# Kernel tuning notes

Hardware: AMD Instinct MI355X
Metric: run time of the kernel (lower is better)

Reference implementation:

```python
import jax, jax.numpy as jnp
import numpy as np

B, P, G, C = 32, 8192, 150, 8
ALPHA, GAMMA, W_ASPECT = 0.25, 2.0, 1.0
THRESH = 1.5          # current_epoch = 0  (< 5)
COST_W_DIST, COST_W_CLS = 2.0, 0.5  # current_epoch < 10
EPS = 1e-6


def _boxes(key, shape):
    k1, k2 = jax.random.split(key)
    c = jax.random.uniform(k1, shape + (2,), minval=0.1, maxval=0.9)
    s = jax.random.uniform(k2, shape + (2,), minval=0.01, maxval=0.2)
    return jnp.concatenate([c - s / 2, c + s / 2], axis=-1)  # valid xyxy


def setup_inputs() -> dict:
    key = jax.random.key(0)
    ks = jax.random.split(key, 6)
    return {
        "pred_objectness": jax.random.uniform(ks[0], (B, P), dtype=jnp.float32),
        "pred_bboxes": _boxes(ks[1], (B, P)),
        "pred_class_logits": jax.random.normal(ks[2], (B, P, C), dtype=jnp.float32),
        "gt_bboxes": _boxes(ks[3], (B, G)),
        "gt_labels": jax.random.randint(ks[4], (B, G), 0, C),
        "num_objects": jax.random.randint(ks[5], (B,), 1, G),
    }


def _giou(b1, b2):
    # elementwise over broadcastable [..., 4] boxes
    a1 = (b1[..., 2] - b1[..., 0]) * (b1[..., 3] - b1[..., 1])
    a2 = (b2[..., 2] - b2[..., 0]) * (b2[..., 3] - b2[..., 1])
    iw = jnp.clip(jnp.minimum(b1[..., 2], b2[..., 2]) - jnp.maximum(b1[..., 0], b2[..., 0]), 0.0)
    ih = jnp.clip(jnp.minimum(b1[..., 3], b2[..., 3]) - jnp.maximum(b1[..., 1], b2[..., 1]), 0.0)
    inter = iw * ih
    union = a1 + a2 - inter
    iou = inter / (union + EPS)
    enc = (jnp.maximum(b1[..., 2], b2[..., 2]) - jnp.minimum(b1[..., 0], b2[..., 0])) * \
          (jnp.maximum(b1[..., 3], b2[..., 3]) - jnp.minimum(b1[..., 1], b2[..., 1]))
    return iou - (enc - union) / (enc + EPS)


def _focal(p, t):
    p = jnp.clip(p, 1e-7, 1.0 - 1e-7)
    bce = -(t * jnp.log(p) + (1.0 - t) * jnp.log(1.0 - p))
    pt = p * t + (1.0 - p) * (1.0 - t)
    return jnp.mean(ALPHA * (1.0 - pt) ** GAMMA * bce)


def _per_image(obj, pbox, plog, gbox, glbl, n_obj):
    gt_mask = jnp.arange(G) < n_obj                              # [G]
    pc = (pbox[:, :2] + pbox[:, 2:]) / 2
    gc = (gbox[:, :2] + gbox[:, 2:]) / 2
    d2 = jnp.sum((pc[:, None, :] - gc[None, :, :]) ** 2, axis=-1)  # [P,G]
    norm_dist = jnp.sqrt(jnp.clip(d2, 1e-12)) / jnp.sqrt(2.0)
    giou_m = _giou(pbox[:, None, :], gbox[None, :, :])           # [P,G]
    probs = jax.nn.softmax(plog, axis=-1)                        # [P,C]
    cls_cost = -probs[:, glbl]                                   # [P,G]
    cost = COST_W_DIST * norm_dist - giou_m + COST_W_CLS * cls_cost
    min_cost = cost.min(axis=0)                                  # per-gt best pred
    assigned = cost.argmin(axis=0)                               # [G]
    valid = (min_cost < THRESH) & gt_mask
    # conflict resolution: for each pred, keep the lowest-cost gt assigned to it
    M = valid[None, :] & (assigned[None, :] == jnp.arange(P)[:, None])  # [P,G]
    matched = M.any(axis=1)                                      # [P]
    best_gt = jnp.where(M, cost, jnp.inf).argmin(axis=1)         # [P]
    wm = matched.astype(cost.dtype)
    n_m = wm.sum()
    denom = jnp.maximum(n_m, 1.0)
    obj_loss = _focal(obj, wm)
    mg = gbox[best_gt]                                           # [P,4]
    giou_loss = jnp.sum(wm * (1.0 - _giou(pbox, mg))) / denom
    pa = (pbox[:, 2] - pbox[:, 0]) / (pbox[:, 3] - pbox[:, 1] + EPS)
    ga = (mg[:, 2] - mg[:, 0]) / (mg[:, 3] - mg[:, 1] + EPS)
    da = jnp.abs(pa - ga)
    sl1 = jnp.where(da < 1.0, 0.5 * da * da, da - 0.5)
    aspect_loss = jnp.sum(wm * sl1) / denom
    lsm = jax.nn.log_softmax(plog, axis=-1)
    ce = -lsm[jnp.arange(P), glbl[best_gt]]
    class_loss = jnp.sum(wm * ce) / denom
    return obj_loss, giou_loss + W_ASPECT * aspect_loss, class_loss, n_m


def reference(pred_objectness, pred_bboxes, pred_class_logits, gt_bboxes, gt_labels, num_objects):
    o, bb, cl, nm = jax.vmap(_per_image)(pred_objectness, pred_bboxes, pred_class_logits,
                                         gt_bboxes, gt_labels, num_objects)
    denom = jnp.maximum(nm.sum(), 1.0)
    obj_loss = o.mean()
    bbox_loss = bb.sum() / denom
    class_loss = cl.sum() / denom
    total_loss = obj_loss + bbox_loss + class_loss
    return total_loss, obj_loss, bbox_loss, class_loss
```

## Files before the change

kernel.cpp:

```cpp
#include <hip/hip_runtime.h>
#include <math.h>

namespace {
constexpr int B_ = 32, P_ = 8192, G_ = 150, C_ = 8;
constexpr int TG = 10;
constexpr int NTILE = G_ / TG;
constexpr int PCH = 16;
constexpr int PCHUNK = P_ / PCH;
constexpr int NXCD = 8;
constexpr int LT = 1024;
constexpr float ALPHA_ = 0.25f;
constexpr float THRESH_ = 1.5f;
constexpr float EPS_ = 1e-6f;
constexpr float LOG2E_ = 1.44269504088896340736f;
constexpr float LN2_   = 0.69314718055994530942f;
constexpr float HSQ2_ = 0.70710678118654752440f;
}

__device__ __forceinline__ float rcp_f(float x) { return __builtin_amdgcn_rcpf(x); }
__device__ __forceinline__ float rfl_f(float x) {
    return __int_as_float(__builtin_amdgcn_readfirstlane(__float_as_int(x)));
}

__device__ __forceinline__ float giou_f(const float4 b1, const float4 b2) {
    float a1 = (b1.z - b1.x) * (b1.w - b1.y);
    float a2 = (b2.z - b2.x) * (b2.w - b2.y);
    float iw = fmaxf(fminf(b1.z, b2.z) - fmaxf(b1.x, b2.x), 0.0f);
    float ih = fmaxf(fminf(b1.w, b2.w) - fmaxf(b1.y, b2.y), 0.0f);
    float inter = iw * ih;
    float uni = a1 + a2 - inter;
    float iou = inter / (uni + EPS_);
    float enc = (fmaxf(b1.z, b2.z) - fminf(b1.x, b2.x)) *
                (fmaxf(b1.w, b2.w) - fminf(b1.y, b2.y));
    return iou - (enc - uni) / (enc + EPS_);
}

__device__ __forceinline__ float block_sum1024(float v, const int tid) {
    __shared__ float tmp[LT / 64];
    for (int off = 32; off; off >>= 1) v += __shfl_down(v, off, 64);
    if ((tid & 63) == 0) tmp[tid >> 6] = v;
    __syncthreads();
    float r = 0.0f;
#pragma unroll
    for (int i = 0; i < LT / 64; ++i) r += tmp[i];
    __syncthreads();
    return r;
}

__global__ __launch_bounds__(64) void k_cost_min(
    const float* __restrict__ pbox,
    const float* __restrict__ plog,
    const float* __restrict__ gbox,
    const int*   __restrict__ glbl,
    const int*   __restrict__ nobj,
    float* __restrict__ out_minc,
    int*   __restrict__ out_assig,
    int*   __restrict__ cnt)
{
    if (blockIdx.x == 0 && threadIdx.x == 0) *cnt = 0;

    const int bid  = blockIdx.x;
    const int xcd  = bid & (NXCD - 1);
    const int t2   = bid >> 3;
    const int tile = t2 % NTILE;
    const int grp  = t2 / NTILE;
    const int pair = xcd + NXCD * grp;
    const int ch   = pair & (PCH - 1);
    const int b    = pair >> 4;
    const int g0   = tile * TG;
    if (g0 >= nobj[b]) return;

    const int tid = threadIdx.x;
    const int p0  = ch * PCHUNK;

    __shared__ float sw[64][9];

    float gx1[TG], gy1[TG], gx2[TG], gy2[TG], gcx[TG], gcy[TG], gar[TG];
    int gL[TG];
    {
        const float4* gb4 = (const float4*)(gbox + ((size_t)b * G_ + g0) * 4);
        const int* gl = glbl + b * G_ + g0;
#pragma unroll
        for (int j = 0; j < TG; ++j) {
            const float4 gb = gb4[j];
            gx1[j] = rfl_f(gb.x); gy1[j] = rfl_f(gb.y);
            gx2[j] = rfl_f(gb.z); gy2[j] = rfl_f(gb.w);
            gcx[j] = rfl_f((gb.x + gb.z) * HSQ2_);
            gcy[j] = rfl_f((gb.y + gb.w) * HSQ2_);
            gar[j] = rfl_f((gb.z - gb.x) * (gb.w - gb.y));
            gL[j]  = __builtin_amdgcn_readfirstlane(gl[j]);
        }
    }

    float bc[TG]; int bi[TG];
#pragma unroll
    for (int j = 0; j < TG; ++j) { bc[j] = INFINITY; bi[j] = 0; }

    const float4* pb4 = (const float4*)(pbox + (size_t)b * P_ * 4);
    const float4* pl4 = (const float4*)(plog + (size_t)b * P_ * C_);

    for (int p = p0 + tid; p < p0 + PCHUNK; p += 64) {
        const float4 pb = pb4[p];
        const float4 l0 = pl4[2 * p];
        const float4 l1 = pl4[2 * p + 1];
        const float pcx = (pb.x + pb.z) * HSQ2_;
        const float pcy = (pb.y + pb.w) * HSQ2_;
        const float a1  = (pb.z - pb.x) * (pb.w - pb.y);

        const float m = fmaxf(fmaxf(fmaxf(l0.x, l0.y), fmaxf(l0.z, l0.w)),
                              fmaxf(fmaxf(l1.x, l1.y), fmaxf(l1.z, l1.w)));
        const float mm = -m * LOG2E_;
        const float e0 = __builtin_amdgcn_exp2f(fmaf(l0.x, LOG2E_, mm));
        const float e1 = __builtin_amdgcn_exp2f(fmaf(l0.y, LOG2E_, mm));
        const float e2 = __builtin_amdgcn_exp2f(fmaf(l0.z, LOG2E_, mm));
        const float e3 = __builtin_amdgcn_exp2f(fmaf(l0.w, LOG2E_, mm));
        const float e4 = __builtin_amdgcn_exp2f(fmaf(l1.x, LOG2E_, mm));
        const float e5 = __builtin_amdgcn_exp2f(fmaf(l1.y, LOG2E_, mm));
        const float e6 = __builtin_amdgcn_exp2f(fmaf(l1.z, LOG2E_, mm));
        const float e7 = __builtin_amdgcn_exp2f(fmaf(l1.w, LOG2E_, mm));
        const float se = ((e0 + e1) + (e2 + e3)) + ((e4 + e5) + (e6 + e7));
        const float s  = -0.5f * rcp_f(se);
        sw[tid][0] = e0 * s; sw[tid][1] = e1 * s; sw[tid][2] = e2 * s; sw[tid][3] = e3 * s;
        sw[tid][4] = e4 * s; sw[tid][5] = e5 * s; sw[tid][6] = e6 * s; sw[tid][7] = e7 * s;

#pragma unroll
        for (int j = 0; j < TG; ++j) {
            const float dx = pcx - gcx[j], dy = pcy - gcy[j];
            const float d2 = fmaf(dx, dx, dy * dy);
            const float sd = __builtin_amdgcn_sqrtf(d2);

            const float iwr = fminf(pb.z, gx2[j]) - fmaxf(pb.x, gx1[j]);
            const float ihr = fminf(pb.w, gy2[j]) - fmaxf(pb.y, gy1[j]);
            const float inter = fmaxf(iwr, 0.0f) * fmaxf(ihr, 0.0f);
            const float uni = (a1 + gar[j]) - inter;
            const float encw = (fmaxf(pb.z, gx2[j]) - fminf(pb.x, gx1[j]));
            const float ench = (fmaxf(pb.w, gy2[j]) - fminf(pb.y, gy1[j]));
            const float enc  = encw * ench;
            const float x = uni + EPS_;
            const float y = enc + EPS_;
            const float r = rcp_f(x * y);
            const float num = fmaf(enc - uni, x, -(inter * y));
            const float c0 = num * r;
            const float cost = sd + (c0 + sw[tid][gL[j]]);
            if (cost < bc[j]) { bc[j] = cost; bi[j] = p; }
        }
    }

#pragma unroll
    for (int j = 0; j < TG; ++j) {
        float c = bc[j]; int i = bi[j];
        for (int off = 32; off; off >>= 1) {
            const float c2 = __shfl_down(c, off, 64);
            const int   i2 = __shfl_down(i, off, 64);
            if (c2 < c || (c2 == c && i2 < i)) { c = c2; i = i2; }
        }
        if (tid == 0) {
            out_minc[(b * G_ + g0 + j) * PCH + ch]  = c;
            out_assig[(b * G_ + g0 + j) * PCH + ch] = i;
        }
    }
}

__global__ __launch_bounds__(LT) void k_losses(
    const float* __restrict__ obj,
    const float* __restrict__ pbox,
    const float* __restrict__ plog,
    const float* __restrict__ gbox,
    const int*   __restrict__ glbl,
    const int*   __restrict__ nobj,
    const float* __restrict__ pminc,
    const int*   __restrict__ passig,
    float* __restrict__ img,
    int* __restrict__ cnt,
    float* __restrict__ out)
{
    const int b = blockIdx.x, tid = threadIdx.x;
    __shared__ float s_c[G_];
    __shared__ int   s_p[G_];
    __shared__ unsigned char s_valid[G_], s_win[G_];
    __shared__ int s_wp[G_], s_wg[G_], s_nw;
    __shared__ int s_last;

    const int n = nobj[b];
    if (tid < G_) {
        float c = INFINITY; int i = 0x7fffffff;
        const float* pc = pminc  + (size_t)(b * G_ + tid) * PCH;
        const int*   pi = passig + (size_t)(b * G_ + tid) * PCH;
#pragma unroll
        for (int ch = 0; ch < PCH; ++ch) {
            const float c2 = pc[ch]; const int i2 = pi[ch];
            if (c2 < c || (c2 == c && i2 < i)) { c = c2; i = i2; }
        }
        s_c[tid] = c;
        s_p[tid] = i;
        s_valid[tid] = (c < THRESH_) && (tid < n);
    }
    __syncthreads();

    if (tid < G_) {
        unsigned char w = 0;
        if (s_valid[tid]) {
            w = 1;
            const int p = s_p[tid]; const float c = s_c[tid];
            for (int g2 = 0; g2 < G_; ++g2) {
                if (g2 == tid || !s_valid[g2] || s_p[g2] != p) continue;
                const float c2 = s_c[g2];
                if (c2 < c || (c2 == c && g2 < tid)) { w = 0; break; }
            }
        }
        s_win[tid] = w;
    }
    __syncthreads();
    if (tid == 0) {
        int nw = 0;
        for (int g = 0; g < G_; ++g) nw += s_win[g];
        s_nw = nw;
    }
    if (tid < G_ && s_win[tid]) {
        int slot = 0;
        for (int g2 = 0; g2 < tid; ++g2) slot += s_win[g2];
        s_wp[slot] = s_p[tid];
        s_wg[slot] = tid;
    }
    __syncthreads();
    const int nw = s_nw;

    const float* ob = obj + (size_t)b * P_;
    float fsum = 0.0f;
#pragma unroll
    for (int k = 0; k < P_ / LT; ++k) {
        float v = ob[tid + k * LT];
        v = fminf(fmaxf(v, 1e-7f), 1.0f - 1e-7f);
        const float nl = -__builtin_amdgcn_logf(1.0f - v) * LN2_;
        fsum += ALPHA_ * v * v * nl;
    }

    float gsum = 0.0f, asum = 0.0f, csum = 0.0f;
    if (tid < nw) {
        const int p = s_wp[tid], g = s_wg[tid];
        float v = ob[p];
        v = fminf(fmaxf(v, 1e-7f), 1.0f - 1e-7f);
        const float nl1 = -__builtin_amdgcn_logf(1.0f - v) * LN2_;
        fsum += ALPHA_ * (1.0f - v) * (1.0f - v) * (-logf(v))
              - ALPHA_ * v * v * nl1;

        const float4 pb = *(const float4*)(pbox + ((size_t)b * P_ + p) * 4);
        const float4 gb = *(const float4*)(gbox + ((size_t)b * G_ + g) * 4);
        gsum = 1.0f - giou_f(pb, gb);

        const float pa = (pb.z - pb.x) / (pb.w - pb.y + EPS_);
        const float ga = (gb.z - gb.x) / (gb.w - gb.y + EPS_);
        const float da = fabsf(pa - ga);
        asum = (da < 1.0f) ? 0.5f * da * da : (da - 0.5f);

        const float* lg = plog + ((size_t)b * P_ + p) * C_;
        const float l0 = lg[0], l1 = lg[1], l2 = lg[2], l3 = lg[3];
        const float l4 = lg[4], l5 = lg[5], l6 = lg[6], l7 = lg[7];
        const float m = fmaxf(fmaxf(fmaxf(l0, l1), fmaxf(l2, l3)),
                              fmaxf(fmaxf(l4, l5), fmaxf(l6, l7)));
        const float se = expf(l0 - m) + expf(l1 - m) + expf(l2 - m) + expf(l3 - m)
                       + expf(l4 - m) + expf(l5 - m) + expf(l6 - m) + expf(l7 - m);
        const int L = glbl[b * G_ + g];
        const float lL = lg[L];
        csum = -(lL - m - logf(se));
    }

    const float ft  = block_sum1024(fsum, tid);
    const float gt_ = block_sum1024(gsum, tid);
    const float at  = block_sum1024(asum, tid);
    const float ct  = block_sum1024(csum, tid);

    if (tid == 0) {
        const float denom = fmaxf((float)nw, 1.0f);
        img[b * 4 + 0] = ft / (float)P_;
        img[b * 4 + 1] = gt_ / denom + at / denom;
        img[b * 4 + 2] = ct / denom;
        img[b * 4 + 3] = (float)nw;
        __threadfence();
        const int old = atomicAdd(cnt, 1);
        s_last = (old == B_ - 1);
    }
    __syncthreads();
    if (tid == 0 && s_last) {
        __threadfence();
        float so = 0.f, sbb = 0.f, scl = 0.f, snm = 0.f;
        for (int bb2 = 0; bb2 < B_; ++bb2) {
            so  += img[bb2 * 4 + 0];
            sbb += img[bb2 * 4 + 1];
            scl += img[bb2 * 4 + 2];
            snm += img[bb2 * 4 + 3];
        }
        const float denom = fmaxf(snm, 1.0f);
        const float o  = so / (float)B_;
        const float bb = sbb / denom;
        const float cl = scl / denom;
        out[0] = o + bb + cl;
        out[1] = o;
        out[2] = bb;
        out[3] = cl;
        *cnt = 0;
    }
}

extern "C" void kernel_launch(void* const* d_in, const int* in_sizes, int n_in,
                              void* d_out, int out_size, void* d_ws, size_t ws_size,
                              hipStream_t stream) {
    const float* obj  = (const float*)d_in[0];
    const float* pbox = (const float*)d_in[1];
    const float* plog = (const float*)d_in[2];
    const float* gbox = (const float*)d_in[3];
    const int*   glbl = (const int*)d_in[4];
    const int*   nobj = (const int*)d_in[5];
    float* out = (float*)d_out;

    char* ws = (char*)d_ws;
    size_t off = 0;
    float* pminc  = (float*)(ws + off); off += (size_t)B_ * G_ * PCH * 4;
    int*   passig = (int*)  (ws + off); off += (size_t)B_ * G_ * PCH * 4;
    float* img    = (float*)(ws + off); off += (size_t)B_ * 4 * 4;
    int*   cnt    = (int*)  (ws + off); off += 64;

    k_cost_min<<<dim3(NTILE * PCH * B_), 64, 0, stream>>>(pbox, plog, gbox, glbl,
                                                          nobj, pminc, passig, cnt);
    k_losses<<<dim3(B_), LT, 0, stream>>>(obj, pbox, plog, gbox, glbl, nobj,
                                          pminc, passig, img, cnt, out);
}
```

Baseline: 75.68 us.

## Parallelize winner resolution, fuse block reductions, vectorize objectness loads in loss kernel

The loss kernel drops from 1024 to 512 threads per block. The serial 150-way per-GT conflict scan is split across 8 sub-slices per GT, and the winning GTs are recorded in a shared bitmask, so slot prefix sums use popcount instead of linear loops. The four separate block reductions become one float4 reduction with a single sync pair, and objectness values are read as float4. The goal is to shorten the serial, single-thread parts of this single-wave-per-image kernel. The cost is an extra barrier and shared atomics.

```diff
diff --git a/kernel.cpp b/kernel.cpp
--- a/kernel.cpp
+++ b/kernel.cpp
@@ -8,7 +8,7 @@
 constexpr int PCH = 16;
 constexpr int PCHUNK = P_ / PCH;
 constexpr int NXCD = 8;
-constexpr int LT = 1024;
+constexpr int LT = 512;
 constexpr float ALPHA_ = 0.25f;
 constexpr float THRESH_ = 1.5f;
 constexpr float EPS_ = 1e-6f;
@@ -35,15 +35,24 @@
     return iou - (enc - uni) / (enc + EPS_);
 }
 
-__device__ __forceinline__ float block_sum1024(float v, const int tid) {
-    __shared__ float tmp[LT / 64];
-    for (int off = 32; off; off >>= 1) v += __shfl_down(v, off, 64);
-    if ((tid & 63) == 0) tmp[tid >> 6] = v;
-    __syncthreads();
-    float r = 0.0f;
-#pragma unroll
-    for (int i = 0; i < LT / 64; ++i) r += tmp[i];
-    __syncthreads();
+__device__ __forceinline__ float4 block_sum4(float4 v, const int tid) {
+    __shared__ float tmp[LT / 64][4];
+    for (int o = 32; o; o >>= 1) {
+        v.x += __shfl_down(v.x, o, 64);
+        v.y += __shfl_down(v.y, o, 64);
+        v.z += __shfl_down(v.z, o, 64);
+        v.w += __shfl_down(v.w, o, 64);
+    }
+    const int wv = tid >> 6;
+    if ((tid & 63) == 0) {
+        tmp[wv][0] = v.x; tmp[wv][1] = v.y; tmp[wv][2] = v.z; tmp[wv][3] = v.w;
+    }
+    __syncthreads();
+    float4 r = make_float4(0.f, 0.f, 0.f, 0.f);
+#pragma unroll
+    for (int i = 0; i < LT / 64; ++i) {
+        r.x += tmp[i][0]; r.y += tmp[i][1]; r.z += tmp[i][2]; r.w += tmp[i][3];
+    }
     return r;
 }
 
@@ -177,12 +186,15 @@
     const int b = blockIdx.x, tid = threadIdx.x;
     __shared__ float s_c[G_];
     __shared__ int   s_p[G_];
-    __shared__ unsigned char s_valid[G_], s_win[G_];
+    __shared__ unsigned char s_valid[G_], s_beat[G_];
+    __shared__ unsigned int s_winm[5];
     __shared__ int s_wp[G_], s_wg[G_], s_nw;
     __shared__ int s_last;
 
     const int n = nobj[b];
+    if (tid < 5) s_winm[tid] = 0;
     if (tid < G_) {
+        s_beat[tid] = 0;
         float c = INFINITY; int i = 0x7fffffff;
         const float* pc = pminc  + (size_t)(b * G_ + tid) * PCH;
         const int*   pi = passig + (size_t)(b * G_ + tid) * PCH;
@@ -197,28 +209,38 @@
     }
     __syncthreads();
 
+    for (int t = tid; t < G_ * 8; t += LT) {
+        const int g  = t >> 3;
+        const int sl = t & 7;
+        if (!s_valid[g]) continue;
+        const int p = s_p[g]; const float c = s_c[g];
+        const int g2e = min(sl * 19 + 19, G_);
+        for (int g2 = sl * 19; g2 < g2e; ++g2) {
+            if (g2 == g || !s_valid[g2] || s_p[g2] != p) continue;
+            const float c2 = s_c[g2];
+            if (c2 < c || (c2 == c && g2 < g)) { s_beat[g] = 1; break; }
+        }
+    }
+    __syncthreads();
+
     if (tid < G_) {
-        unsigned char w = 0;
-        if (s_valid[tid]) {
-            w = 1;
-            const int p = s_p[tid]; const float c = s_c[tid];
-            for (int g2 = 0; g2 < G_; ++g2) {
-                if (g2 == tid || !s_valid[g2] || s_p[g2] != p) continue;
-                const float c2 = s_c[g2];
-                if (c2 < c || (c2 == c && g2 < tid)) { w = 0; break; }
-            }
-        }
-        s_win[tid] = w;
-    }
-    __syncthreads();
+        if (s_valid[tid] && !s_beat[tid])
+            atomicOr(&s_winm[tid >> 5], 1u << (tid & 31));
+    }
+    __syncthreads();
+
     if (tid == 0) {
         int nw = 0;
-        for (int g = 0; g < G_; ++g) nw += s_win[g];
+#pragma unroll
+        for (int w2 = 0; w2 < 5; ++w2) nw += __popc(s_winm[w2]);
         s_nw = nw;
     }
-    if (tid < G_ && s_win[tid]) {
-        int slot = 0;
-        for (int g2 = 0; g2 < tid; ++g2) slot += s_win[g2];
+    if (tid < G_ && s_valid[tid] && !s_beat[tid]) {
+        const int word = tid >> 5, bit = tid & 31;
+        int slot = __popc(s_winm[word] & ((1u << bit) - 1));
+#pragma unroll
+        for (int w2 = 0; w2 < 4; ++w2)
+            if (w2 < word) slot += __popc(s_winm[w2]);
         s_wp[slot] = s_p[tid];
         s_wg[slot] = tid;
     }
@@ -226,13 +248,18 @@
     const int nw = s_nw;
 
     const float* ob = obj + (size_t)b * P_;
+    const float4* ob4 = (const float4*)ob;
     float fsum = 0.0f;
 #pragma unroll
-    for (int k = 0; k < P_ / LT; ++k) {
-        float v = ob[tid + k * LT];
-        v = fminf(fmaxf(v, 1e-7f), 1.0f - 1e-7f);
-        const float nl = -__builtin_amdgcn_logf(1.0f - v) * LN2_;
-        fsum += ALPHA_ * v * v * nl;
+    for (int k = 0; k < P_ / (LT * 4); ++k) {
+        const float4 v4 = ob4[tid + k * LT];
+        const float vs[4] = {v4.x, v4.y, v4.z, v4.w};
+#pragma unroll
+        for (int u = 0; u < 4; ++u) {
+            float v = fminf(fmaxf(vs[u], 1e-7f), 1.0f - 1e-7f);
+            const float nl = -__builtin_amdgcn_logf(1.0f - v) * LN2_;
+            fsum += ALPHA_ * v * v * nl;
+        }
     }
 
     float gsum = 0.0f, asum = 0.0f, csum = 0.0f;
@@ -265,16 +292,13 @@
         csum = -(lL - m - logf(se));
     }
 
-    const float ft  = block_sum1024(fsum, tid);
-    const float gt_ = block_sum1024(gsum, tid);
-    const float at  = block_sum1024(asum, tid);
-    const float ct  = block_sum1024(csum, tid);
+    const float4 tot = block_sum4(make_float4(fsum, gsum, asum, csum), tid);
 
     if (tid == 0) {
         const float denom = fmaxf((float)nw, 1.0f);
-        img[b * 4 + 0] = ft / (float)P_;
-        img[b * 4 + 1] = gt_ / denom + at / denom;
-        img[b * 4 + 2] = ct / denom;
+        img[b * 4 + 0] = tot.x / (float)P_;
+        img[b * 4 + 1] = tot.y / denom + tot.z / denom;
+        img[b * 4 + 2] = tot.w / denom;
         img[b * 4 + 3] = (float)nw;
         __threadfence();
         const int old = atomicAdd(cnt, 1);
```

Result: faster. 62.24 us (-17.8%).
